# Kernel optimization log

Measured on AMD Instinct MI355X. Metric: run time of the kernel, lower is better.

## Reference

```python
import jax, jax.numpy as jnp
import numpy as np

Q_DEFAULT = 8
XI_MAX = 0.4          # center frequency of the highest-frequency wavelet (cycles/sample)
BW_RATIO = 0.8        # bandwidth-to-center-frequency ratio
LOG_EPS = 1e-6


def _make_filters(T, Q):
    """Morlet-style analytic filter bank in the Fourier domain (all static numpy)."""
    J = int(np.floor(np.log2(T / 2)))
    freqs = np.fft.fftfreq(T).astype(np.float32)          # [T], in [-0.5, 0.5)
    # first-order wavelets: J*Q filters, geometrically spaced, quality factor Q
    n1 = J * Q
    xi1 = (XI_MAX * 2.0 ** (-np.arange(n1) / Q)).astype(np.float32)
    sig1 = (BW_RATIO * xi1 / Q).astype(np.float32)
    psi1 = np.exp(-(freqs[None, :] - xi1[:, None]) ** 2 / (2.0 * sig1[:, None] ** 2)).astype(np.float32)  # [n1, T]
    # second-order wavelets: Q2 = 1, one per octave
    xi2 = (XI_MAX * 2.0 ** (-np.arange(J))).astype(np.float32)
    sig2 = (BW_RATIO * xi2).astype(np.float32)
    psi2 = np.exp(-(freqs[None, :] - xi2[:, None]) ** 2 / (2.0 * sig2[:, None] ** 2)).astype(np.float32)  # [J, T]
    # low-pass (phi): Gaussian at scale 2^J
    sigma_phi = np.float32(BW_RATIO * XI_MAX * 2.0 ** (-J))
    phi = np.exp(-(freqs ** 2) / (2.0 * sigma_phi ** 2)).astype(np.float32)  # [T]
    # valid second-order paths: xi2 strictly below xi1 (frequency-decreasing cascade)
    pair_j1, pair_k = [], []
    for k in range(J):
        for j1 in range(n1):
            if xi2[k] < xi1[j1]:
                pair_j1.append(j1)
                pair_k.append(k)
    return psi1, psi2, phi, np.asarray(pair_j1, np.int32), np.asarray(pair_k, np.int32)


def _scatter(x_flat, psi1, psi2, phi, pair_j1, pair_k):
    """x_flat: [N, T] real. Returns S: [N, 1 + n1 + n_pairs, T]."""
    xh = jnp.fft.fft(x_flat)                                   # [N, T] complex
    S0 = jnp.fft.ifft(xh * phi).real[:, None, :]               # order 0 (dropped later)
    U1 = jnp.abs(jnp.fft.ifft(xh[:, None, :] * psi1[None]))    # [N, n1, T]
    U1h = jnp.fft.fft(U1)
    S1 = jnp.fft.ifft(U1h * phi).real                          # [N, n1, T]
    U2 = jnp.abs(jnp.fft.ifft(U1h[:, pair_j1, :] * psi2[pair_k][None]))  # [N, P, T]
    S2 = jnp.fft.ifft(jnp.fft.fft(U2) * phi).real              # [N, P, T]
    return jnp.concatenate([S0, S1, S2], axis=1)


def setup_inputs() -> dict:
    key = jax.random.key(0)
    x = jax.random.normal(key, (8, 2048, 6), dtype=jnp.float32)
    return {"x": x}


def reference(x):
    B, T, C = x.shape
    psi1, psi2, phi, pj, pk = _make_filters(T, Q_DEFAULT)
    psi1, psi2, phi = jnp.asarray(psi1), jnp.asarray(psi2), jnp.asarray(phi)
    # vectorize the original per-channel Python loop: fold channels into batch
    xf = jnp.transpose(x, (0, 2, 1)).reshape(B * C, T)          # [B*C, T]
    S = _scatter(xf, psi1, psi2, phi, pj, pk)                   # [B*C, n_coef+1, T]
    out = jnp.mean(jnp.log(S[:, 1:, :] + LOG_EPS), axis=-1)     # drop order-0, log, time-mean
    return out.reshape(B, C, -1).transpose(0, 2, 1)             # [B, n_coef, C]
```

## Files before the change

### kernel.cpp

```cpp
#include <hip/hip_runtime.h>

#define NTH 256

#define PHI1 0.29504296f
#define PHI2 0.0075683594f
#define GCUT 18.0f

__device__ __forceinline__ int swz(int i) { return i ^ (((i >> 4) & 3) * 5); }

__device__ __forceinline__ float2 cmul(float2 a, float2 b) {
  return make_float2(a.x * b.x - a.y * b.y, a.x * b.y + a.y * b.x);
}

template <int W>
__device__ __forceinline__ float wsum(float v) {
#pragma unroll
  for (int off = 1; off < W; off <<= 1) v += __shfl_xor(v, off, 64);
  return v;
}

template <int M>
__device__ __forceinline__ int prevM(int i) {
  if (M == 128)
    return ((i >> 5) & 3) | (((i >> 3) & 3) << 2) | (((i >> 1) & 3) << 4) | ((i & 1) << 6);
  else if (M == 256)
    return ((i & 3) << 6) | (((i >> 2) & 3) << 4) | (((i >> 4) & 3) << 2) | ((i >> 6) & 3);
  else if (M == 512)
    return ((i >> 7) & 3) | (((i >> 5) & 3) << 2) | (((i >> 3) & 3) << 4) |
           (((i >> 1) & 3) << 6) | ((i & 1) << 8);
  else if (M == 1024)
    return ((i >> 8) & 3) | (((i >> 6) & 3) << 2) | (((i >> 4) & 3) << 4) |
           (((i >> 2) & 3) << 6) | ((i & 3) << 8);
  else
    return ((i >> 9) & 3) | (((i >> 7) & 3) << 2) | (((i >> 5) & 3) << 4) |
           (((i >> 3) & 3) << 6) | (((i >> 1) & 3) << 8) | ((i & 1) << 10);
}

template <bool INV>
__device__ __forceinline__ void dif4(float2* A, int j, int ls, float astep) {
  const int s = 1 << ls;
  const int e = j & (s - 1);
  const int base = ((j >> ls) << (ls + 2)) | e;
  float2 w1;
  __sincosf(astep * (float)e, &w1.y, &w1.x);
  if (INV) w1.y = -w1.y;
  const float2 w2 = cmul(w1, w1);
  const float2 w3 = cmul(w2, w1);
  const float2 a0 = A[swz(base)];
  const float2 a1 = A[swz(base + s)];
  const float2 a2 = A[swz(base + 2 * s)];
  const float2 a3 = A[swz(base + 3 * s)];
  const float t0x = a0.x + a2.x, t0y = a0.y + a2.y;
  const float t1x = a0.x - a2.x, t1y = a0.y - a2.y;
  const float t2x = a1.x + a3.x, t2y = a1.y + a3.y;
  const float bdx = a1.x - a3.x, bdy = a1.y - a3.y;
  const float sgn = INV ? -1.0f : 1.0f;
  const float t3x = sgn * bdy, t3y = -sgn * bdx;
  A[swz(base)]         = make_float2(t0x + t2x, t0y + t2y);
  A[swz(base + s)]     = cmul(make_float2(t1x + t3x, t1y + t3y), w1);
  A[swz(base + 2 * s)] = cmul(make_float2(t0x - t2x, t0y - t2y), w2);
  A[swz(base + 3 * s)] = cmul(make_float2(t1x - t3x, t1y - t3y), w3);
}

__device__ __forceinline__ void dit4(float2* A, int j, int ls, float astep) {
  const int s = 1 << ls;
  const int e = j & (s - 1);
  const int base = ((j >> ls) << (ls + 2)) | e;
  float2 w1;
  __sincosf(astep * (float)e, &w1.y, &w1.x);
  const float2 w2 = cmul(w1, w1);
  const float2 w3 = cmul(w2, w1);
  const float2 c0 = A[swz(base)];
  const float2 c1 = cmul(A[swz(base + s)], w1);
  const float2 c2 = cmul(A[swz(base + 2 * s)], w2);
  const float2 c3 = cmul(A[swz(base + 3 * s)], w3);
  const float t0x = c0.x + c2.x, t0y = c0.y + c2.y;
  const float t1x = c0.x - c2.x, t1y = c0.y - c2.y;
  const float t2x = c1.x + c3.x, t2y = c1.y + c3.y;
  const float bdx = c1.x - c3.x, bdy = c1.y - c3.y;
  const float t3x = bdy, t3y = -bdx;
  A[swz(base)]         = make_float2(t0x + t2x, t0y + t2y);
  A[swz(base + s)]     = make_float2(t1x + t3x, t1y + t3y);
  A[swz(base + 2 * s)] = make_float2(t0x - t2x, t0y - t2y);
  A[swz(base + 3 * s)] = make_float2(t1x - t3x, t1y - t3y);
}

__device__ __forceinline__ void r2pair(float2* A, int g) {
  const float2 a = A[swz(2 * g)];
  const float2 b = A[swz(2 * g + 1)];
  A[swz(2 * g)]     = make_float2(a.x + b.x, a.y + b.y);
  A[swz(2 * g + 1)] = make_float2(a.x - b.x, a.y - b.y);
}

template <int M> struct LMof { static constexpr int v =
  (M == 2048) ? 11 : (M == 1024) ? 10 : (M == 512) ? 9 : (M == 256) ? 8 : 7; };

template <int M, bool INV>
__device__ __forceinline__ void dif_blk(float2* A) {
  constexpr int LM = LMof<M>::v;
  constexpr int NB = M / 4;
  const int tid = (int)threadIdx.x;
#pragma unroll
  for (int ls = LM - 2; ls >= (LM & 1); ls -= 2) {
    const float astep = -1.5707963267948966f / (float)(1 << ls);
    __syncthreads();
#pragma unroll
    for (int i = 0; i < NB / NTH; ++i) dif4<INV>(A, tid + NTH * i, ls, astep);
  }
  if (LM & 1) {
    __syncthreads();
#pragma unroll
    for (int i = 0; i < (M / 2) / NTH; ++i) r2pair(A, tid + NTH * i);
  }
  __syncthreads();
}

template <int M>
__device__ __forceinline__ void dit_blk(float2* A) {
  constexpr int LM = LMof<M>::v;
  constexpr int NB = M / 4;
  const int tid = (int)threadIdx.x;
  if (LM & 1) {
    __syncthreads();
#pragma unroll
    for (int i = 0; i < (M / 2) / NTH; ++i) r2pair(A, tid + NTH * i);
  }
#pragma unroll
  for (int ls = (LM & 1); ls <= LM - 2; ls += 2) {
    const float astep = -1.5707963267948966f / (float)(1 << ls);
    __syncthreads();
#pragma unroll
    for (int i = 0; i < NB / NTH; ++i) dit4(A, tid + NTH * i, ls, astep);
  }
  __syncthreads();
}

template <int M, bool INV, int LANES>
__device__ __forceinline__ void dif_w(float2* Aw, int l) {
  constexpr int LM = LMof<M>::v;
  constexpr int NB = M / 4;
#pragma unroll
  for (int ls = LM - 2; ls >= (LM & 1); ls -= 2) {
    const float astep = -1.5707963267948966f / (float)(1 << ls);
#pragma unroll
    for (int i = 0; i < NB / LANES; ++i) dif4<INV>(Aw, l + LANES * i, ls, astep);
  }
  if (LM & 1) {
#pragma unroll
    for (int i = 0; i < (M / 2) / LANES; ++i) r2pair(Aw, l + LANES * i);
  }
}

template <int M, int LANES>
__device__ __forceinline__ void dit_w(float2* Aw, int l) {
  constexpr int LM = LMof<M>::v;
  constexpr int NB = M / 4;
  if (LM & 1) {
#pragma unroll
    for (int i = 0; i < (M / 2) / LANES; ++i) r2pair(Aw, l + LANES * i);
  }
#pragma unroll
  for (int ls = (LM & 1); ls <= LM - 2; ls += 2) {
    const float astep = -1.5707963267948966f / (float)(1 << ls);
#pragma unroll
    for (int i = 0; i < NB / LANES; ++i) dit4(Aw, l + LANES * i, ls, astep);
  }
}

__global__ __launch_bounds__(NTH) void kA(const float* __restrict__ x,
                                          float2* __restrict__ xh) {
  __shared__ float2 A[2048];
  const int n = blockIdx.x, b = n / 6, c = n % 6;
  const float* xp = x + (size_t)b * (2048 * 6) + c;
#pragma unroll
  for (int i = 0; i < 8; ++i) {
    const int t = (int)threadIdx.x + NTH * i;
    A[swz(t)] = make_float2(xp[t * 6], 0.0f);
  }
  dif_blk<2048, false>(A);
#pragma unroll
  for (int i = 0; i < 8; ++i) {
    const int t = (int)threadIdx.x + NTH * i;
    xh[(size_t)n * 2048 + prevM<2048>(t)] = A[swz(t)];
  }
}


__device__ __noinline__ void parent_blk1024(const float2* __restrict__ src,
                                            float* __restrict__ outp, int j1) {
  extern __shared__ float2 L[];
  float2* A = L;
  float* scr = (float*)(L + 3968);
  constexpr int M1 = 1024;
  constexpr int NR = 4;
  const int tid = (int)threadIdx.x;
  const float xi = 0.4f * exp2f(-0.125f * (float)j1);
  const float sig = 0.1f * xi;
  const float i2s = 1.0f / (2.0f * sig * sig);
#pragma unroll
  for (int i = 0; i < NR; ++i) {
    const int m = tid + NTH * i;
    float2 acc = make_float2(0.0f, 0.0f);
#pragma unroll
    for (int q = 0; q < 2; ++q) {
      const int f = m + q * M1;
      const float fr = (float)(f < 1024 ? f : f - 2048) * (1.0f / 2048.0f);
      const float d = fr - xi;
      const float dd = d * d * i2s;
      if (dd < GCUT) {
        const float g = __expf(-dd);
        const float2 v = src[f];
        acc.x += v.x * g; acc.y += v.y * g;
      }
    }
    A[swz(m)] = acc;
  }
  dif_blk<M1, true>(A);
#pragma unroll
  for (int i = 0; i < NR; ++i) {
    const int m = tid + NTH * i;
    const float2 zv = A[swz(m)];
    A[swz(m)] = make_float2(sqrtf(zv.x * zv.x + zv.y * zv.y) * (1.0f / 2048.0f), 0.0f);
  }
  dit_blk<M1>(A);
  const float invM = 1.0f / (float)M1;
  const float c0 = A[0].x * invM;
  const float2 U1 = A[1], U2 = A[2];
  const float k1 = PHI1 * 2.0f * invM, k2 = PHI2 * 2.0f * invM;
  float part = 0.0f;
#pragma unroll
  for (int i = 0; i < NR; ++i) {
    const int t = tid + NTH * i;
    float sv, cv;
    __sincosf((6.283185307179586f / (float)M1) * (float)t, &sv, &cv);
    float acc = c0 + k1 * (U1.x * cv - U1.y * sv);
    const float c2 = cv * cv - sv * sv, s2 = 2.0f * sv * cv;
    acc += k2 * (U2.x * c2 - U2.y * s2);
    part += __logf(acc + 1e-6f);
  }
  part = wsum<64>(part);
  const int lane = tid & 63, wid = tid >> 6;
  if (lane == 0) scr[wid] = part;
  __syncthreads();
  if (tid == 0) *outp = (scr[0] + scr[1] + scr[2] + scr[3]) * invM;
}

template <int M1>
__device__ __noinline__ void parent_wav(int aoff, const float2* __restrict__ src,
                                        float* __restrict__ outp, int j1, int l) {
  extern __shared__ float2 L[];
  float2* Aw = L + aoff;
  constexpr int NRW = M1 / 64;
  constexpr int F = 2048 / M1;
  const float xi = 0.4f * exp2f(-0.125f * (float)j1);
  const float sig = 0.1f * xi;
  const float i2s = 1.0f / (2.0f * sig * sig);
#pragma unroll
  for (int i = 0; i < NRW; ++i) {
    const int m = l + 64 * i;
    float2 acc = make_float2(0.0f, 0.0f);
#pragma unroll
    for (int q = 0; q < F; ++q) {
      const int f = m + q * M1;
      const float fr = (float)(f < 1024 ? f : f - 2048) * (1.0f / 2048.0f);
      const float d = fr - xi;
      const float dd = d * d * i2s;
      if (dd < GCUT) {
        const float g = __expf(-dd);
        const float2 v = src[f];
        acc.x += v.x * g; acc.y += v.y * g;
      }
    }
    Aw[swz(m)] = acc;
  }
  dif_w<M1, true, 64>(Aw, l);
#pragma unroll
  for (int i = 0; i < NRW; ++i) {
    const int m = l + 64 * i;
    const float2 zv = Aw[swz(m)];
    Aw[swz(m)] = make_float2(sqrtf(zv.x * zv.x + zv.y * zv.y) * (1.0f / 2048.0f), 0.0f);
  }
  dit_w<M1, 64>(Aw, l);
  const float invM = 1.0f / (float)M1;
  const float c0 = Aw[0].x * invM;
  const float2 U1 = Aw[1], U2 = Aw[2];
  const float k1 = PHI1 * 2.0f * invM, k2 = PHI2 * 2.0f * invM;
  float part = 0.0f;
#pragma unroll
  for (int i = 0; i < NRW; ++i) {
    const int t = l + 64 * i;
    float sv, cv;
    __sincosf((6.283185307179586f / (float)M1) * (float)t, &sv, &cv);
    float acc = c0 + k1 * (U1.x * cv - U1.y * sv);
    const float c2 = cv * cv - sv * sv, s2 = 2.0f * sv * cv;
    acc += k2 * (U2.x * c2 - U2.y * s2);
    part += __logf(acc + 1e-6f);
  }
  part = wsum<64>(part);
  if (l == 0) *outp = part * invM;
}

__device__ __noinline__ void parent_dual(int aoff, const float2* __restrict__ src,
                                         float* __restrict__ outp, int j1, int ll) {
  extern __shared__ float2 L[];
  float2* Ah = L + aoff;
  const float xi = 0.4f * exp2f(-0.125f * (float)j1);
  const float sig = 0.1f * xi;
  const float i2s = 1.0f / (2.0f * sig * sig);
#pragma unroll
  for (int i = 0; i < 4; ++i) {
    const int m = ll + 32 * i;
    float2 acc = make_float2(0.0f, 0.0f);
#pragma unroll
    for (int q = 0; q < 16; ++q) {
      const int f = m + q * 128;
      const float fr = (float)(f < 1024 ? f : f - 2048) * (1.0f / 2048.0f);
      const float d = fr - xi;
      const float dd = d * d * i2s;
      if (dd < GCUT) {
        const float g = __expf(-dd);
        const float2 v = src[f];
        acc.x += v.x * g; acc.y += v.y * g;
      }
    }
    Ah[swz(m)] = acc;
  }
  dif_w<128, true, 32>(Ah, ll);
#pragma unroll
  for (int i = 0; i < 4; ++i) {
    const int m = ll + 32 * i;
    const float2 zv = Ah[swz(m)];
    Ah[swz(m)] = make_float2(sqrtf(zv.x * zv.x + zv.y * zv.y) * (1.0f / 2048.0f), 0.0f);
  }
  dit_w<128, 32>(Ah, ll);
  const float invM = 1.0f / 128.0f;
  const float c0 = Ah[0].x * invM;
  const float2 U1 = Ah[1], U2 = Ah[2];
  const float k1 = PHI1 * 2.0f * invM, k2 = PHI2 * 2.0f * invM;
  float part = 0.0f;
#pragma unroll
  for (int i = 0; i < 4; ++i) {
    const int t = ll + 32 * i;
    float sv, cv;
    __sincosf((6.283185307179586f / 128.0f) * (float)t, &sv, &cv);
    float acc = c0 + k1 * (U1.x * cv - U1.y * sv);
    const float c2 = cv * cv - sv * sv, s2 = 2.0f * sv * cv;
    acc += k2 * (U2.x * c2 - U2.y * s2);
    part += __logf(acc + 1e-6f);
  }
  part = wsum<32>(part);
  if (ll == 0) *outp = part * invM;
}

template <int M2>
__device__ __noinline__ void desc_wav(int aoff, int voff, float* __restrict__ outp,
                                      int M1, int F, float xi, int l) {
  extern __shared__ float2 L[];
  float2* Aw = L + aoff;
  const float2* Vl = L + voff;
  constexpr int NR2 = M2 / 64;
  const float sg = 0.8f * xi;
  const float i2s = 1.0f / (2.0f * sg * sg);
#pragma unroll
  for (int ii = 0; ii < NR2; ++ii) {
    const int m = l + 64 * ii;
    float2 acc = make_float2(0.0f, 0.0f);
    for (int q = 0; q < F; ++q) {
      const int f = m + q * M2;
      const float fr = (float)(f < (M1 >> 1) ? f : f - M1) * (1.0f / 2048.0f);
      const float d = fr - xi;
      const float dd = d * d * i2s;
      if (dd < GCUT) {
        const float g = __expf(-dd);
        const float2 vv = Vl[swz(f)];
        acc.x += vv.x * g; acc.y += vv.y * g;
      }
    }
    Aw[swz(m)] = acc;
  }
  dif_w<M2, true, 64>(Aw, l);
  const float invM1f = 1.0f / (float)M1;
  float b0 = 0, b1r = 0, b1i = 0, b2r = 0, b2i = 0;
#pragma unroll
  for (int ii = 0; ii < NR2; ++ii) {
    const int idx = l + 64 * ii;
    const float2 zv = Aw[swz(idx)];
    const float u = sqrtf(zv.x * zv.x + zv.y * zv.y) * invM1f;
    const int t = prevM<M2>(idx);
    float sv, cv;
    __sincosf((6.283185307179586f / (float)M2) * (float)t, &sv, &cv);
    b0 += u;
    b1r += u * cv; b1i -= u * sv;
    const float c2 = cv * cv - sv * sv, s2 = 2.0f * sv * cv;
    b2r += u * c2; b2i -= u * s2;
  }
  b0 = wsum<64>(b0);
  b1r = wsum<64>(b1r); b1i = wsum<64>(b1i);
  b2r = wsum<64>(b2r); b2i = wsum<64>(b2i);
  const float k1 = 2.0f * PHI1, k2 = 2.0f * PHI2;
  const float invM2 = 1.0f / (float)M2;
  float part = 0.0f;
#pragma unroll
  for (int ii = 0; ii < NR2; ++ii) {
    const int idx = l + 64 * ii;
    const int t = prevM<M2>(idx);
    float sv, cv;
    __sincosf((6.283185307179586f / (float)M2) * (float)t, &sv, &cv);
    float acc = b0 + k1 * (b1r * cv - b1i * sv);
    const float c2 = cv * cv - sv * sv, s2 = 2.0f * sv * cv;
    acc += k2 * (b2r * c2 - b2i * s2);
    part += __logf(acc * invM2 + 1e-6f);
  }
  part = wsum<64>(part);
  if (l == 0) *outp = part * invM2;
}

__device__ __noinline__ void desc_dual(int aoff, int voff, float* __restrict__ outp,
                                       int M1, int F, float xi, int ll) {
  extern __shared__ float2 L[];
  float2* Ah = L + aoff;
  const float2* Vl = L + voff;
  const float sg = 0.8f * xi;
  const float i2s = 1.0f / (2.0f * sg * sg);
#pragma unroll
  for (int ii = 0; ii < 4; ++ii) {
    const int m = ll + 32 * ii;
    float2 acc = make_float2(0.0f, 0.0f);
    for (int q = 0; q < F; ++q) {
      const int f = m + q * 128;
      const float fr = (float)(f < (M1 >> 1) ? f : f - M1) * (1.0f / 2048.0f);
      const float d = fr - xi;
      const float dd = d * d * i2s;
      if (dd < GCUT) {
        const float g = __expf(-dd);
        const float2 vv = Vl[swz(f)];
        acc.x += vv.x * g; acc.y += vv.y * g;
      }
    }
    Ah[swz(m)] = acc;
  }
  dif_w<128, true, 32>(Ah, ll);
  const float invM1f = 1.0f / (float)M1;
  float b0 = 0, b1r = 0, b1i = 0, b2r = 0, b2i = 0;
#pragma unroll
  for (int ii = 0; ii < 4; ++ii) {
    const int idx = ll + 32 * ii;
    const float2 zv = Ah[swz(idx)];
    const float u = sqrtf(zv.x * zv.x + zv.y * zv.y) * invM1f;
    const int t = prevM<128>(idx);
    float sv, cv;
    __sincosf((6.283185307179586f / 128.0f) * (float)t, &sv, &cv);
    b0 += u;
    b1r += u * cv; b1i -= u * sv;
    const float c2 = cv * cv - sv * sv, s2 = 2.0f * sv * cv;
    b2r += u * c2; b2i -= u * s2;
  }
  b0 = wsum<32>(b0);
  b1r = wsum<32>(b1r); b1i = wsum<32>(b1i);
  b2r = wsum<32>(b2r); b2i = wsum<32>(b2i);
  const float k1 = 2.0f * PHI1, k2 = 2.0f * PHI2;
  const float invM2 = 1.0f / 128.0f;
  float part = 0.0f;
#pragma unroll
  for (int ii = 0; ii < 4; ++ii) {
    const int idx = ll + 32 * ii;
    const int t = prevM<128>(idx);
    float sv, cv;
    __sincosf((6.283185307179586f / 128.0f) * (float)t, &sv, &cv);
    float acc = b0 + k1 * (b1r * cv - b1i * sv);
    const float c2 = cv * cv - sv * sv, s2 = 2.0f * sv * cv;
    acc += k2 * (b2r * c2 - b2i * s2);
    part += __logf(acc * invM2 + 1e-6f);
  }
  part = wsum<32>(part);
  if (ll == 0) *outp = part * invM2;
}

__device__ __forceinline__ float* o1p(float* out, int b, int c, int j1) {
  return out + ((size_t)b * 440 + j1) * 6 + c;
}
__device__ __forceinline__ float* o2p(float* out, int b, int c, int j1, int k) {
  return out + ((size_t)b * 440 + 80 + 4 * k * (k - 1) + j1) * 6 + c;
}
__device__ __forceinline__ float xi2f(int k) { return 0.4f * exp2f(-(float)k); }

__global__ __launch_bounds__(NTH, 4) void kBC(const float2* __restrict__ xh,
                                              float* __restrict__ out) {
  extern __shared__ float2 L[];
  const int ci = (int)blockIdx.x / 48;
  const int n  = (int)blockIdx.x % 48;
  const int b = n / 6, c = n % 6;
  const float2* src = xh + (size_t)n * 2048;
  const int tid = (int)threadIdx.x;
  const int wid = tid >> 6, l = tid & 63;
  const int h = l >> 5, ll = l & 31;

  if (ci < 2) {
    const int j1 = 8 + 4 * ci + wid;
    const int a0 = wid * 1024;
    parent_wav<512>(a0, src, o1p(out, b, c, j1), j1, l);
    desc_wav<512>(a0 + 512, a0, o2p(out, b, c, j1, 2), 512, 1, xi2f(2), l);
    desc_wav<256>(a0 + 512, a0, o2p(out, b, c, j1, 3), 512, 2, xi2f(3), l);
    for (int i = 0; i < 3; ++i) {
      const int k = 4 + 2 * i + h;
      desc_dual(a0 + 512 + h * 128, a0, o2p(out, b, c, j1, k), 512, 4, xi2f(k), ll);
    }
  } else if (ci < 4) {
    const int j1 = 16 + 4 * (ci - 2) + wid;
    const int a0 = wid * 512;
    parent_wav<256>(a0, src, o1p(out, b, c, j1), j1, l);
    desc_wav<256>(a0 + 256, a0, o2p(out, b, c, j1, 3), 256, 1, xi2f(3), l);
    for (int i = 0; i < 3; ++i) {
      const int k = 4 + 2 * i + h;
      desc_dual(a0 + 256 + h * 128, a0, o2p(out, b, c, j1, k), 256, 2, xi2f(k), ll);
    }
  } else if (ci < 12) {
    const int j1 = ci - 4;
    parent_blk1024(src, o1p(out, b, c, j1), j1);
    if (wid == 0) {
      desc_wav<1024>(1024, 0, o2p(out, b, c, j1, 1), 1024, 1, xi2f(1), l);
    } else if (wid == 1) {
      desc_wav<512>(2048, 0, o2p(out, b, c, j1, 2), 1024, 2, xi2f(2), l);
      const int k = 5 + h;
      desc_dual(3328 + h * 128, 0, o2p(out, b, c, j1, k), 1024, 8, xi2f(k), ll);
    } else if (wid == 2) {
      desc_wav<512>(2560, 0, o2p(out, b, c, j1, 3), 1024, 2, xi2f(3), l);
      const int k = 7 + h;
      desc_dual(3584 + h * 128, 0, o2p(out, b, c, j1, k), 1024, 8, xi2f(k), ll);
    } else {
      desc_wav<256>(3072, 0, o2p(out, b, c, j1, 4), 1024, 4, xi2f(4), l);
      if (h == 0)
        desc_dual(3840, 0, o2p(out, b, c, j1, 9), 1024, 8, xi2f(9), ll);
    }
  } else {
    const int o = ci - 9;
    const int slot = 2 * wid + h;
    const int j1 = 8 * o + slot;
    const int a0 = slot * 256;
    parent_dual(a0, src, o1p(out, b, c, j1), j1, ll);
    for (int k = o + 1; k <= 9; ++k)
      desc_dual(a0 + 128, a0, o2p(out, b, c, j1, k), 128, 1, xi2f(k), ll);
  }
}

extern "C" void kernel_launch(void* const* d_in, const int* in_sizes, int n_in,
                              void* d_out, int out_size, void* d_ws, size_t ws_size,
                              hipStream_t stream) {
  (void)in_sizes; (void)n_in; (void)out_size; (void)ws_size;
  const float* x = (const float*)d_in[0];
  float* out = (float*)d_out;
  float2* xh = (float2*)d_ws;
  kA<<<dim3(48), dim3(NTH), 0, stream>>>(x, xh);
  kBC<<<dim3(19 * 48), dim3(NTH), 32768, stream>>>(xh, out);
}
```

Baseline: 86.95 us.

## Split scattering into parent and descendant kernels with register-resident shuffle FFTs

Replaces the shared-memory radix-4 FFTs inside the fused second kernel with register-resident FFTs that use in-register butterflies and cross-lane shuffles. The work is split into two kernels: kB computes the first-order wavelet paths and writes U1 spectra to a global workspace, and kC runs each second-order path as its own wave-level task reading from that workspace. This removes shared memory and block barriers and spreads the work across many more blocks to balance load. In exchange it adds a kernel launch and a global round trip for the U1 spectra, and puts more pressure on registers.

```diff
diff --git a/kernel.cpp b/kernel.cpp
--- a/kernel.cpp
+++ b/kernel.cpp
@@ -1,6 +1,7 @@
 #include <hip/hip_runtime.h>
 
 #define NTH 256
+#define U1H_STRIDE 21504
 
 #define PHI1 0.29504296f
 #define PHI2 0.0075683594f
@@ -19,21 +20,75 @@
   return v;
 }
 
-template <int M>
-__device__ __forceinline__ int prevM(int i) {
-  if (M == 128)
-    return ((i >> 5) & 3) | (((i >> 3) & 3) << 2) | (((i >> 1) & 3) << 4) | ((i & 1) << 6);
-  else if (M == 256)
-    return ((i & 3) << 6) | (((i >> 2) & 3) << 4) | (((i >> 4) & 3) << 2) | ((i >> 6) & 3);
-  else if (M == 512)
-    return ((i >> 7) & 3) | (((i >> 5) & 3) << 2) | (((i >> 3) & 3) << 4) |
-           (((i >> 1) & 3) << 6) | ((i & 1) << 8);
-  else if (M == 1024)
-    return ((i >> 8) & 3) | (((i >> 6) & 3) << 2) | (((i >> 4) & 3) << 4) |
-           (((i >> 2) & 3) << 6) | ((i & 3) << 8);
-  else
-    return ((i >> 9) & 3) | (((i >> 7) & 3) << 2) | (((i >> 5) & 3) << 4) |
-           (((i >> 3) & 3) << 6) | (((i >> 1) & 3) << 8) | ((i & 1) << 10);
+__device__ __forceinline__ float2 shflx2(float2 v, int mask) {
+  return make_float2(__shfl_xor(v.x, mask, 64), __shfl_xor(v.y, mask, 64));
+}
+
+template <int M, int LANES, bool INV>
+__device__ __forceinline__ void rdif(float2* x, int l) {
+  constexpr int R = M / LANES;
+#pragma unroll
+  for (int half = R / 2; half >= 1; half >>= 1) {
+    const int s = half * LANES;
+    const float a0 = (INV ? 3.14159265358979f : -3.14159265358979f) / (float)s;
+#pragma unroll
+    for (int r = 0; r < R; ++r) {
+      if ((r & half) == 0) {
+        const float2 a = x[r], b = x[r + half];
+        const int j = (r & (half - 1)) * LANES + l;
+        float2 w; __sincosf(a0 * (float)j, &w.y, &w.x);
+        x[r] = make_float2(a.x + b.x, a.y + b.y);
+        x[r + half] = cmul(make_float2(a.x - b.x, a.y - b.y), w);
+      }
+    }
+  }
+#pragma unroll
+  for (int s = LANES / 2; s >= 1; s >>= 1) {
+    const float a0 = (INV ? 3.14159265358979f : -3.14159265358979f) / (float)s;
+    float2 w; __sincosf(a0 * (float)(l & (s - 1)), &w.y, &w.x);
+    const bool hi = (l & s) != 0;
+#pragma unroll
+    for (int r = 0; r < R; ++r) {
+      const float2 y = shflx2(x[r], s);
+      const float2 sum = make_float2(x[r].x + y.x, x[r].y + y.y);
+      const float2 dif = cmul(make_float2(y.x - x[r].x, y.y - x[r].y), w);
+      x[r] = hi ? dif : sum;
+    }
+  }
+}
+
+template <int M, int LANES, bool INV>
+__device__ __forceinline__ void rdit(float2* x, int l) {
+  constexpr int R = M / LANES;
+#pragma unroll
+  for (int s = 1; s <= LANES / 2; s <<= 1) {
+    const float a0 = (INV ? 3.14159265358979f : -3.14159265358979f) / (float)s;
+    float2 w; __sincosf(a0 * (float)(l & (s - 1)), &w.y, &w.x);
+    const bool hi = (l & s) != 0;
+#pragma unroll
+    for (int r = 0; r < R; ++r) {
+      const float2 y = shflx2(x[r], s);
+      const float2 wb = cmul(w, hi ? x[r] : y);
+      x[r] = hi ? make_float2(y.x - wb.x, y.y - wb.y)
+                : make_float2(x[r].x + wb.x, x[r].y + wb.y);
+    }
+  }
+#pragma unroll
+  for (int half = 1; half <= R / 2; half <<= 1) {
+    const int s = half * LANES;
+    const float a0 = (INV ? 3.14159265358979f : -3.14159265358979f) / (float)s;
+#pragma unroll
+    for (int r = 0; r < R; ++r) {
+      if ((r & half) == 0) {
+        const int j = (r & (half - 1)) * LANES + l;
+        float2 w; __sincosf(a0 * (float)j, &w.y, &w.x);
+        const float2 bw = cmul(x[r + half], w);
+        const float2 a = x[r];
+        x[r] = make_float2(a.x + bw.x, a.y + bw.y);
+        x[r + half] = make_float2(a.x - bw.x, a.y - bw.y);
+      }
+    }
+  }
 }
 
 template <bool INV>
@@ -62,29 +117,6 @@
   A[swz(base + 3 * s)] = cmul(make_float2(t1x - t3x, t1y - t3y), w3);
 }
 
-__device__ __forceinline__ void dit4(float2* A, int j, int ls, float astep) {
-  const int s = 1 << ls;
-  const int e = j & (s - 1);
-  const int base = ((j >> ls) << (ls + 2)) | e;
-  float2 w1;
-  __sincosf(astep * (float)e, &w1.y, &w1.x);
-  const float2 w2 = cmul(w1, w1);
-  const float2 w3 = cmul(w2, w1);
-  const float2 c0 = A[swz(base)];
-  const float2 c1 = cmul(A[swz(base + s)], w1);
-  const float2 c2 = cmul(A[swz(base + 2 * s)], w2);
-  const float2 c3 = cmul(A[swz(base + 3 * s)], w3);
-  const float t0x = c0.x + c2.x, t0y = c0.y + c2.y;
-  const float t1x = c0.x - c2.x, t1y = c0.y - c2.y;
-  const float t2x = c1.x + c3.x, t2y = c1.y + c3.y;
-  const float bdx = c1.x - c3.x, bdy = c1.y - c3.y;
-  const float t3x = bdy, t3y = -bdx;
-  A[swz(base)]         = make_float2(t0x + t2x, t0y + t2y);
-  A[swz(base + s)]     = make_float2(t1x + t3x, t1y + t3y);
-  A[swz(base + 2 * s)] = make_float2(t0x - t2x, t0y - t2y);
-  A[swz(base + 3 * s)] = make_float2(t1x - t3x, t1y - t3y);
-}
-
 __device__ __forceinline__ void r2pair(float2* A, int g) {
   const float2 a = A[swz(2 * g)];
   const float2 b = A[swz(2 * g + 1)];
@@ -92,79 +124,9 @@
   A[swz(2 * g + 1)] = make_float2(a.x - b.x, a.y - b.y);
 }
 
-template <int M> struct LMof { static constexpr int v =
-  (M == 2048) ? 11 : (M == 1024) ? 10 : (M == 512) ? 9 : (M == 256) ? 8 : 7; };
-
-template <int M, bool INV>
-__device__ __forceinline__ void dif_blk(float2* A) {
-  constexpr int LM = LMof<M>::v;
-  constexpr int NB = M / 4;
-  const int tid = (int)threadIdx.x;
-#pragma unroll
-  for (int ls = LM - 2; ls >= (LM & 1); ls -= 2) {
-    const float astep = -1.5707963267948966f / (float)(1 << ls);
-    __syncthreads();
-#pragma unroll
-    for (int i = 0; i < NB / NTH; ++i) dif4<INV>(A, tid + NTH * i, ls, astep);
-  }
-  if (LM & 1) {
-    __syncthreads();
-#pragma unroll
-    for (int i = 0; i < (M / 2) / NTH; ++i) r2pair(A, tid + NTH * i);
-  }
-  __syncthreads();
-}
-
-template <int M>
-__device__ __forceinline__ void dit_blk(float2* A) {
-  constexpr int LM = LMof<M>::v;
-  constexpr int NB = M / 4;
-  const int tid = (int)threadIdx.x;
-  if (LM & 1) {
-    __syncthreads();
-#pragma unroll
-    for (int i = 0; i < (M / 2) / NTH; ++i) r2pair(A, tid + NTH * i);
-  }
-#pragma unroll
-  for (int ls = (LM & 1); ls <= LM - 2; ls += 2) {
-    const float astep = -1.5707963267948966f / (float)(1 << ls);
-    __syncthreads();
-#pragma unroll
-    for (int i = 0; i < NB / NTH; ++i) dit4(A, tid + NTH * i, ls, astep);
-  }
-  __syncthreads();
-}
-
-template <int M, bool INV, int LANES>
-__device__ __forceinline__ void dif_w(float2* Aw, int l) {
-  constexpr int LM = LMof<M>::v;
-  constexpr int NB = M / 4;
-#pragma unroll
-  for (int ls = LM - 2; ls >= (LM & 1); ls -= 2) {
-    const float astep = -1.5707963267948966f / (float)(1 << ls);
-#pragma unroll
-    for (int i = 0; i < NB / LANES; ++i) dif4<INV>(Aw, l + LANES * i, ls, astep);
-  }
-  if (LM & 1) {
-#pragma unroll
-    for (int i = 0; i < (M / 2) / LANES; ++i) r2pair(Aw, l + LANES * i);
-  }
-}
-
-template <int M, int LANES>
-__device__ __forceinline__ void dit_w(float2* Aw, int l) {
-  constexpr int LM = LMof<M>::v;
-  constexpr int NB = M / 4;
-  if (LM & 1) {
-#pragma unroll
-    for (int i = 0; i < (M / 2) / LANES; ++i) r2pair(Aw, l + LANES * i);
-  }
-#pragma unroll
-  for (int ls = (LM & 1); ls <= LM - 2; ls += 2) {
-    const float astep = -1.5707963267948966f / (float)(1 << ls);
-#pragma unroll
-    for (int i = 0; i < NB / LANES; ++i) dit4(Aw, l + LANES * i, ls, astep);
-  }
+__device__ __forceinline__ int prev2048(int i) {
+  return ((i >> 9) & 3) | (((i >> 7) & 3) << 2) | (((i >> 5) & 3) << 4) |
+         (((i >> 3) & 3) << 6) | (((i >> 1) & 3) << 8) | ((i & 1) << 10);
 }
 
 __global__ __launch_bounds__(NTH) void kA(const float* __restrict__ x,
@@ -177,87 +139,56 @@
     const int t = (int)threadIdx.x + NTH * i;
     A[swz(t)] = make_float2(xp[t * 6], 0.0f);
   }
-  dif_blk<2048, false>(A);
+  const int tid = (int)threadIdx.x;
+#pragma unroll
+  for (int ls = 9; ls >= 1; ls -= 2) {
+    const float astep = -1.5707963267948966f / (float)(1 << ls);
+    __syncthreads();
+#pragma unroll
+    for (int i = 0; i < 2; ++i) dif4<false>(A, tid + NTH * i, ls, astep);
+  }
+  __syncthreads();
+#pragma unroll
+  for (int i = 0; i < 4; ++i) r2pair(A, tid + NTH * i);
+  __syncthreads();
 #pragma unroll
   for (int i = 0; i < 8; ++i) {
     const int t = (int)threadIdx.x + NTH * i;
-    xh[(size_t)n * 2048 + prevM<2048>(t)] = A[swz(t)];
-  }
-}
-
-
-__device__ __noinline__ void parent_blk1024(const float2* __restrict__ src,
-                                            float* __restrict__ outp, int j1) {
-  extern __shared__ float2 L[];
-  float2* A = L;
-  float* scr = (float*)(L + 3968);
-  constexpr int M1 = 1024;
-  constexpr int NR = 4;
-  const int tid = (int)threadIdx.x;
+    xh[(size_t)n * 2048 + prev2048(t)] = A[swz(t)];
+  }
+}
+
+__device__ __forceinline__ int u1h_off(int j1) {
+  const int o = j1 >> 3;
+  if (o == 0) return j1 * 1024;
+  if (o == 1) return 8192 + (j1 - 8) * 512;
+  if (o == 2) return 12288 + (j1 - 16) * 256;
+  return 14336 + (j1 - 24) * 128;
+}
+__device__ __forceinline__ float* o1p(float* out, int b, int c, int j1) {
+  return out + ((size_t)b * 440 + j1) * 6 + c;
+}
+__device__ __forceinline__ float* o2p(float* out, int b, int c, int j1, int k) {
+  return out + ((size_t)b * 440 + 80 + 4 * k * (k - 1) + j1) * 6 + c;
+}
+__device__ __forceinline__ float xi2f(int k) { return 0.4f * exp2f(-(float)k); }
+
+template <int M1, int LANES>
+__device__ __forceinline__ void parentR(const float2* __restrict__ src,
+                                        float2* __restrict__ Vg,
+                                        float* __restrict__ outp,
+                                        int j1, int lane) {
+  constexpr int R = M1 / LANES;
+  constexpr int F = 2048 / M1;
+  const int l = lane & (LANES - 1);
+  const int gb = lane - l;
   const float xi = 0.4f * exp2f(-0.125f * (float)j1);
   const float sig = 0.1f * xi;
   const float i2s = 1.0f / (2.0f * sig * sig);
-#pragma unroll
-  for (int i = 0; i < NR; ++i) {
-    const int m = tid + NTH * i;
-    float2 acc = make_float2(0.0f, 0.0f);
-#pragma unroll
-    for (int q = 0; q < 2; ++q) {
-      const int f = m + q * M1;
-      const float fr = (float)(f < 1024 ? f : f - 2048) * (1.0f / 2048.0f);
-      const float d = fr - xi;
-      const float dd = d * d * i2s;
-      if (dd < GCUT) {
-        const float g = __expf(-dd);
-        const float2 v = src[f];
-        acc.x += v.x * g; acc.y += v.y * g;
-      }
-    }
-    A[swz(m)] = acc;
-  }
-  dif_blk<M1, true>(A);
-#pragma unroll
-  for (int i = 0; i < NR; ++i) {
-    const int m = tid + NTH * i;
-    const float2 zv = A[swz(m)];
-    A[swz(m)] = make_float2(sqrtf(zv.x * zv.x + zv.y * zv.y) * (1.0f / 2048.0f), 0.0f);
-  }
-  dit_blk<M1>(A);
-  const float invM = 1.0f / (float)M1;
-  const float c0 = A[0].x * invM;
-  const float2 U1 = A[1], U2 = A[2];
-  const float k1 = PHI1 * 2.0f * invM, k2 = PHI2 * 2.0f * invM;
-  float part = 0.0f;
-#pragma unroll
-  for (int i = 0; i < NR; ++i) {
-    const int t = tid + NTH * i;
-    float sv, cv;
-    __sincosf((6.283185307179586f / (float)M1) * (float)t, &sv, &cv);
-    float acc = c0 + k1 * (U1.x * cv - U1.y * sv);
-    const float c2 = cv * cv - sv * sv, s2 = 2.0f * sv * cv;
-    acc += k2 * (U2.x * c2 - U2.y * s2);
-    part += __logf(acc + 1e-6f);
-  }
-  part = wsum<64>(part);
-  const int lane = tid & 63, wid = tid >> 6;
-  if (lane == 0) scr[wid] = part;
-  __syncthreads();
-  if (tid == 0) *outp = (scr[0] + scr[1] + scr[2] + scr[3]) * invM;
-}
-
-template <int M1>
-__device__ __noinline__ void parent_wav(int aoff, const float2* __restrict__ src,
-                                        float* __restrict__ outp, int j1, int l) {
-  extern __shared__ float2 L[];
-  float2* Aw = L + aoff;
-  constexpr int NRW = M1 / 64;
-  constexpr int F = 2048 / M1;
-  const float xi = 0.4f * exp2f(-0.125f * (float)j1);
-  const float sig = 0.1f * xi;
-  const float i2s = 1.0f / (2.0f * sig * sig);
-#pragma unroll
-  for (int i = 0; i < NRW; ++i) {
-    const int m = l + 64 * i;
+  float2 x[R];
+#pragma unroll
+  for (int r = 0; r < R; ++r) {
+    const int m = r * LANES + l;
     float2 acc = make_float2(0.0f, 0.0f);
 #pragma unroll
     for (int q = 0; q < F; ++q) {
@@ -271,24 +202,24 @@
         acc.x += v.x * g; acc.y += v.y * g;
       }
     }
-    Aw[swz(m)] = acc;
-  }
-  dif_w<M1, true, 64>(Aw, l);
-#pragma unroll
-  for (int i = 0; i < NRW; ++i) {
-    const int m = l + 64 * i;
-    const float2 zv = Aw[swz(m)];
-    Aw[swz(m)] = make_float2(sqrtf(zv.x * zv.x + zv.y * zv.y) * (1.0f / 2048.0f), 0.0f);
-  }
-  dit_w<M1, 64>(Aw, l);
+    x[r] = acc;
+  }
+  rdif<M1, LANES, true>(x, l);
+#pragma unroll
+  for (int r = 0; r < R; ++r)
+    x[r] = make_float2(sqrtf(x[r].x * x[r].x + x[r].y * x[r].y) * (1.0f / 2048.0f), 0.0f);
+  rdit<M1, LANES, false>(x, l);
+#pragma unroll
+  for (int r = 0; r < R; ++r) Vg[r * LANES + l] = x[r];
   const float invM = 1.0f / (float)M1;
-  const float c0 = Aw[0].x * invM;
-  const float2 U1 = Aw[1], U2 = Aw[2];
+  const float c0 = __shfl(x[0].x, gb, 64) * invM;
+  const float2 U1 = make_float2(__shfl(x[0].x, gb + 1, 64), __shfl(x[0].y, gb + 1, 64));
+  const float2 U2 = make_float2(__shfl(x[0].x, gb + 2, 64), __shfl(x[0].y, gb + 2, 64));
   const float k1 = PHI1 * 2.0f * invM, k2 = PHI2 * 2.0f * invM;
   float part = 0.0f;
 #pragma unroll
-  for (int i = 0; i < NRW; ++i) {
-    const int t = l + 64 * i;
+  for (int r = 0; r < R; ++r) {
+    const int t = r * LANES + l;
     float sv, cv;
     __sincosf((6.283185307179586f / (float)M1) * (float)t, &sv, &cv);
     float acc = c0 + k1 * (U1.x * cv - U1.y * sv);
@@ -296,74 +227,51 @@
     acc += k2 * (U2.x * c2 - U2.y * s2);
     part += __logf(acc + 1e-6f);
   }
-  part = wsum<64>(part);
+  part = wsum<LANES>(part);
   if (l == 0) *outp = part * invM;
 }
 
-__device__ __noinline__ void parent_dual(int aoff, const float2* __restrict__ src,
-                                         float* __restrict__ outp, int j1, int ll) {
-  extern __shared__ float2 L[];
-  float2* Ah = L + aoff;
-  const float xi = 0.4f * exp2f(-0.125f * (float)j1);
-  const float sig = 0.1f * xi;
-  const float i2s = 1.0f / (2.0f * sig * sig);
-#pragma unroll
-  for (int i = 0; i < 4; ++i) {
-    const int m = ll + 32 * i;
-    float2 acc = make_float2(0.0f, 0.0f);
-#pragma unroll
-    for (int q = 0; q < 16; ++q) {
-      const int f = m + q * 128;
-      const float fr = (float)(f < 1024 ? f : f - 2048) * (1.0f / 2048.0f);
-      const float d = fr - xi;
-      const float dd = d * d * i2s;
-      if (dd < GCUT) {
-        const float g = __expf(-dd);
-        const float2 v = src[f];
-        acc.x += v.x * g; acc.y += v.y * g;
-      }
-    }
-    Ah[swz(m)] = acc;
-  }
-  dif_w<128, true, 32>(Ah, ll);
-#pragma unroll
-  for (int i = 0; i < 4; ++i) {
-    const int m = ll + 32 * i;
-    const float2 zv = Ah[swz(m)];
-    Ah[swz(m)] = make_float2(sqrtf(zv.x * zv.x + zv.y * zv.y) * (1.0f / 2048.0f), 0.0f);
-  }
-  dit_w<128, 32>(Ah, ll);
-  const float invM = 1.0f / 128.0f;
-  const float c0 = Ah[0].x * invM;
-  const float2 U1 = Ah[1], U2 = Ah[2];
-  const float k1 = PHI1 * 2.0f * invM, k2 = PHI2 * 2.0f * invM;
-  float part = 0.0f;
-#pragma unroll
-  for (int i = 0; i < 4; ++i) {
-    const int t = ll + 32 * i;
-    float sv, cv;
-    __sincosf((6.283185307179586f / 128.0f) * (float)t, &sv, &cv);
-    float acc = c0 + k1 * (U1.x * cv - U1.y * sv);
-    const float c2 = cv * cv - sv * sv, s2 = 2.0f * sv * cv;
-    acc += k2 * (U2.x * c2 - U2.y * s2);
-    part += __logf(acc + 1e-6f);
-  }
-  part = wsum<32>(part);
-  if (ll == 0) *outp = part * invM;
-}
-
-template <int M2>
-__device__ __noinline__ void desc_wav(int aoff, int voff, float* __restrict__ outp,
-                                      int M1, int F, float xi, int l) {
-  extern __shared__ float2 L[];
-  float2* Aw = L + aoff;
-  const float2* Vl = L + voff;
-  constexpr int NR2 = M2 / 64;
+__global__ __launch_bounds__(NTH, 4) void kB(const float2* __restrict__ xh,
+                                             float2* __restrict__ U1h,
+                                             float* __restrict__ out) {
+  const int ci = (int)blockIdx.x / 48;
+  const int n  = (int)blockIdx.x % 48;
+  const int b = n / 6, c = n % 6;
+  const float2* src = xh + (size_t)n * 2048;
+  float2* Vb = U1h + (size_t)n * U1H_STRIDE;
+  const int tid = (int)threadIdx.x;
+  const int wid = tid >> 6, lane = tid & 63;
+  const int h = lane >> 5;
+  const int slot = 2 * wid + h;
+
+  if (ci < 2) {
+    const int j1 = 4 * ci + wid;
+    parentR<1024, 64>(src, Vb + u1h_off(j1), o1p(out, b, c, j1), j1, lane);
+  } else if (ci < 4) {
+    const int j1 = 8 + 4 * (ci - 2) + wid;
+    parentR<512, 64>(src, Vb + u1h_off(j1), o1p(out, b, c, j1), j1, lane);
+  } else if (ci < 6) {
+    const int j1 = 16 + 4 * (ci - 4) + wid;
+    parentR<256, 64>(src, Vb + u1h_off(j1), o1p(out, b, c, j1), j1, lane);
+  } else {
+    const int j1 = 24 + 8 * (ci - 6) + slot;
+    parentR<128, 32>(src, Vb + u1h_off(j1), o1p(out, b, c, j1), j1, lane);
+  }
+}
+
+template <int M2, int LANES>
+__device__ __forceinline__ void descR(const float2* __restrict__ Vg,
+                                      float* __restrict__ outp,
+                                      int M1, int F, float xi, int lane) {
+  constexpr int R = M2 / LANES;
+  constexpr int LM = (M2 == 1024) ? 10 : (M2 == 512) ? 9 : (M2 == 256) ? 8 : 7;
+  const int l = lane & (LANES - 1);
   const float sg = 0.8f * xi;
   const float i2s = 1.0f / (2.0f * sg * sg);
-#pragma unroll
-  for (int ii = 0; ii < NR2; ++ii) {
-    const int m = l + 64 * ii;
+  float2 x[R];
+#pragma unroll
+  for (int r = 0; r < R; ++r) {
+    const int m = r * LANES + l;
     float2 acc = make_float2(0.0f, 0.0f);
     for (int q = 0; q < F; ++q) {
       const int f = m + q * M2;
@@ -372,21 +280,20 @@
       const float dd = d * d * i2s;
       if (dd < GCUT) {
         const float g = __expf(-dd);
-        const float2 vv = Vl[swz(f)];
+        const float2 vv = Vg[f];
         acc.x += vv.x * g; acc.y += vv.y * g;
       }
     }
-    Aw[swz(m)] = acc;
-  }
-  dif_w<M2, true, 64>(Aw, l);
+    x[r] = acc;
+  }
+  rdif<M2, LANES, true>(x, l);
   const float invM1f = 1.0f / (float)M1;
   float b0 = 0, b1r = 0, b1i = 0, b2r = 0, b2i = 0;
 #pragma unroll
-  for (int ii = 0; ii < NR2; ++ii) {
-    const int idx = l + 64 * ii;
-    const float2 zv = Aw[swz(idx)];
-    const float u = sqrtf(zv.x * zv.x + zv.y * zv.y) * invM1f;
-    const int t = prevM<M2>(idx);
+  for (int r = 0; r < R; ++r) {
+    const float u = sqrtf(x[r].x * x[r].x + x[r].y * x[r].y) * invM1f;
+    const int e = r * LANES + l;
+    const int t = (int)(__brev((unsigned)e) >> (32 - LM));
     float sv, cv;
     __sincosf((6.283185307179586f / (float)M2) * (float)t, &sv, &cv);
     b0 += u;
@@ -394,16 +301,16 @@
     const float c2 = cv * cv - sv * sv, s2 = 2.0f * sv * cv;
     b2r += u * c2; b2i -= u * s2;
   }
-  b0 = wsum<64>(b0);
-  b1r = wsum<64>(b1r); b1i = wsum<64>(b1i);
-  b2r = wsum<64>(b2r); b2i = wsum<64>(b2i);
+  b0 = wsum<LANES>(b0);
+  b1r = wsum<LANES>(b1r); b1i = wsum<LANES>(b1i);
+  b2r = wsum<LANES>(b2r); b2i = wsum<LANES>(b2i);
   const float k1 = 2.0f * PHI1, k2 = 2.0f * PHI2;
   const float invM2 = 1.0f / (float)M2;
   float part = 0.0f;
 #pragma unroll
-  for (int ii = 0; ii < NR2; ++ii) {
-    const int idx = l + 64 * ii;
-    const int t = prevM<M2>(idx);
+  for (int r = 0; r < R; ++r) {
+    const int e = r * LANES + l;
+    const int t = (int)(__brev((unsigned)e) >> (32 - LM));
     float sv, cv;
     __sincosf((6.283185307179586f / (float)M2) * (float)t, &sv, &cv);
     float acc = b0 + k1 * (b1r * cv - b1i * sv);
@@ -411,135 +318,50 @@
     acc += k2 * (b2r * c2 - b2i * s2);
     part += __logf(acc * invM2 + 1e-6f);
   }
-  part = wsum<64>(part);
+  part = wsum<LANES>(part);
   if (l == 0) *outp = part * invM2;
 }
 
-__device__ __noinline__ void desc_dual(int aoff, int voff, float* __restrict__ outp,
-                                       int M1, int F, float xi, int ll) {
-  extern __shared__ float2 L[];
-  float2* Ah = L + aoff;
-  const float2* Vl = L + voff;
-  const float sg = 0.8f * xi;
-  const float i2s = 1.0f / (2.0f * sg * sg);
-#pragma unroll
-  for (int ii = 0; ii < 4; ++ii) {
-    const int m = ll + 32 * ii;
-    float2 acc = make_float2(0.0f, 0.0f);
-    for (int q = 0; q < F; ++q) {
-      const int f = m + q * 128;
-      const float fr = (float)(f < (M1 >> 1) ? f : f - M1) * (1.0f / 2048.0f);
-      const float d = fr - xi;
-      const float dd = d * d * i2s;
-      if (dd < GCUT) {
-        const float g = __expf(-dd);
-        const float2 vv = Vl[swz(f)];
-        acc.x += vv.x * g; acc.y += vv.y * g;
-      }
-    }
-    Ah[swz(m)] = acc;
-  }
-  dif_w<128, true, 32>(Ah, ll);
-  const float invM1f = 1.0f / (float)M1;
-  float b0 = 0, b1r = 0, b1i = 0, b2r = 0, b2i = 0;
-#pragma unroll
-  for (int ii = 0; ii < 4; ++ii) {
-    const int idx = ll + 32 * ii;
-    const float2 zv = Ah[swz(idx)];
-    const float u = sqrtf(zv.x * zv.x + zv.y * zv.y) * invM1f;
-    const int t = prevM<128>(idx);
-    float sv, cv;
-    __sincosf((6.283185307179586f / 128.0f) * (float)t, &sv, &cv);
-    b0 += u;
-    b1r += u * cv; b1i -= u * sv;
-    const float c2 = cv * cv - sv * sv, s2 = 2.0f * sv * cv;
-    b2r += u * c2; b2i -= u * s2;
-  }
-  b0 = wsum<32>(b0);
-  b1r = wsum<32>(b1r); b1i = wsum<32>(b1i);
-  b2r = wsum<32>(b2r); b2i = wsum<32>(b2i);
-  const float k1 = 2.0f * PHI1, k2 = 2.0f * PHI2;
-  const float invM2 = 1.0f / 128.0f;
-  float part = 0.0f;
-#pragma unroll
-  for (int ii = 0; ii < 4; ++ii) {
-    const int idx = ll + 32 * ii;
-    const int t = prevM<128>(idx);
-    float sv, cv;
-    __sincosf((6.283185307179586f / 128.0f) * (float)t, &sv, &cv);
-    float acc = b0 + k1 * (b1r * cv - b1i * sv);
-    const float c2 = cv * cv - sv * sv, s2 = 2.0f * sv * cv;
-    acc += k2 * (b2r * c2 - b2i * s2);
-    part += __logf(acc * invM2 + 1e-6f);
-  }
-  part = wsum<32>(part);
-  if (ll == 0) *outp = part * invM2;
-}
-
-__device__ __forceinline__ float* o1p(float* out, int b, int c, int j1) {
-  return out + ((size_t)b * 440 + j1) * 6 + c;
-}
-__device__ __forceinline__ float* o2p(float* out, int b, int c, int j1, int k) {
-  return out + ((size_t)b * 440 + 80 + 4 * k * (k - 1) + j1) * 6 + c;
-}
-__device__ __forceinline__ float xi2f(int k) { return 0.4f * exp2f(-(float)k); }
-
-__global__ __launch_bounds__(NTH, 4) void kBC(const float2* __restrict__ xh,
-                                              float* __restrict__ out) {
-  extern __shared__ float2 L[];
+__global__ __launch_bounds__(NTH, 4) void kC(const float2* __restrict__ U1h,
+                                             float* __restrict__ out) {
   const int ci = (int)blockIdx.x / 48;
   const int n  = (int)blockIdx.x % 48;
   const int b = n / 6, c = n % 6;
-  const float2* src = xh + (size_t)n * 2048;
+  const float2* Vb = U1h + (size_t)n * U1H_STRIDE;
   const int tid = (int)threadIdx.x;
-  const int wid = tid >> 6, l = tid & 63;
-  const int h = l >> 5, ll = l & 31;
+  const int wid = tid >> 6, lane = tid & 63;
+  const int h = lane >> 5;
+  const int slot = 2 * wid + h;
 
   if (ci < 2) {
-    const int j1 = 8 + 4 * ci + wid;
-    const int a0 = wid * 1024;
-    parent_wav<512>(a0, src, o1p(out, b, c, j1), j1, l);
-    desc_wav<512>(a0 + 512, a0, o2p(out, b, c, j1, 2), 512, 1, xi2f(2), l);
-    desc_wav<256>(a0 + 512, a0, o2p(out, b, c, j1, 3), 512, 2, xi2f(3), l);
-    for (int i = 0; i < 3; ++i) {
-      const int k = 4 + 2 * i + h;
-      desc_dual(a0 + 512 + h * 128, a0, o2p(out, b, c, j1, k), 512, 4, xi2f(k), ll);
-    }
-  } else if (ci < 4) {
-    const int j1 = 16 + 4 * (ci - 2) + wid;
-    const int a0 = wid * 512;
-    parent_wav<256>(a0, src, o1p(out, b, c, j1), j1, l);
-    desc_wav<256>(a0 + 256, a0, o2p(out, b, c, j1, 3), 256, 1, xi2f(3), l);
-    for (int i = 0; i < 3; ++i) {
-      const int k = 4 + 2 * i + h;
-      desc_dual(a0 + 256 + h * 128, a0, o2p(out, b, c, j1, k), 256, 2, xi2f(k), ll);
-    }
+    const int j1 = 4 * ci + wid;
+    descR<1024, 64>(Vb + u1h_off(j1), o2p(out, b, c, j1, 1), 1024, 1, xi2f(1), lane);
+  } else if (ci < 6) {
+    const int j1 = 4 * (ci - 2) + wid;
+    const int M1 = (j1 < 8) ? 1024 : 512;
+    descR<512, 64>(Vb + u1h_off(j1), o2p(out, b, c, j1, 2), M1, M1 / 512, xi2f(2), lane);
+  } else if (ci < 8) {
+    const int j1 = 4 * (ci - 6) + wid;
+    descR<512, 64>(Vb + u1h_off(j1), o2p(out, b, c, j1, 3), 1024, 2, xi2f(3), lane);
   } else if (ci < 12) {
-    const int j1 = ci - 4;
-    parent_blk1024(src, o1p(out, b, c, j1), j1);
-    if (wid == 0) {
-      desc_wav<1024>(1024, 0, o2p(out, b, c, j1, 1), 1024, 1, xi2f(1), l);
-    } else if (wid == 1) {
-      desc_wav<512>(2048, 0, o2p(out, b, c, j1, 2), 1024, 2, xi2f(2), l);
-      const int k = 5 + h;
-      desc_dual(3328 + h * 128, 0, o2p(out, b, c, j1, k), 1024, 8, xi2f(k), ll);
-    } else if (wid == 2) {
-      desc_wav<512>(2560, 0, o2p(out, b, c, j1, 3), 1024, 2, xi2f(3), l);
-      const int k = 7 + h;
-      desc_dual(3584 + h * 128, 0, o2p(out, b, c, j1, k), 1024, 8, xi2f(k), ll);
-    } else {
-      desc_wav<256>(3072, 0, o2p(out, b, c, j1, 4), 1024, 4, xi2f(4), l);
-      if (h == 0)
-        desc_dual(3840, 0, o2p(out, b, c, j1, 9), 1024, 8, xi2f(9), ll);
-    }
+    const int j1 = 8 + 4 * (ci - 8) + wid;
+    const int M1 = (j1 < 16) ? 512 : 256;
+    descR<256, 64>(Vb + u1h_off(j1), o2p(out, b, c, j1, 3), M1, M1 / 256, xi2f(3), lane);
+  } else if (ci < 14) {
+    const int j1 = 4 * (ci - 12) + wid;
+    descR<256, 64>(Vb + u1h_off(j1), o2p(out, b, c, j1, 4), 1024, 4, xi2f(4), lane);
+  } else if (ci < 17) {
+    const int j1 = 8 + 8 * (ci - 14) + slot;
+    const int o = j1 >> 3;
+    const int M1 = (o < 3) ? (1024 >> o) : 128;
+    descR<128, 32>(Vb + u1h_off(j1), o2p(out, b, c, j1, 4), M1, M1 / 128, xi2f(4), lane);
   } else {
-    const int o = ci - 9;
-    const int slot = 2 * wid + h;
-    const int j1 = 8 * o + slot;
-    const int a0 = slot * 256;
-    parent_dual(a0, src, o1p(out, b, c, j1), j1, ll);
-    for (int k = o + 1; k <= 9; ++k)
-      desc_dual(a0 + 128, a0, o2p(out, b, c, j1, k), 128, 1, xi2f(k), ll);
+    int g = ci - 17;
+    int k = 5;
+    while (g >= k) { g -= k; ++k; }
+    const int j1 = 8 * g + slot;
+    const int M1 = (g < 3) ? (1024 >> g) : 128;
+    descR<128, 32>(Vb + u1h_off(j1), o2p(out, b, c, j1, k), M1, M1 / 128, xi2f(k), lane);
   }
 }
 
@@ -549,7 +371,9 @@
   (void)in_sizes; (void)n_in; (void)out_size; (void)ws_size;
   const float* x = (const float*)d_in[0];
   float* out = (float*)d_out;
-  float2* xh = (float2*)d_ws;
+  float2* U1h = (float2*)d_ws;
+  float2* xh = (float2*)((char*)d_ws + (size_t)48 * U1H_STRIDE * sizeof(float2));
   kA<<<dim3(48), dim3(NTH), 0, stream>>>(x, xh);
-  kBC<<<dim3(19 * 48), dim3(NTH), 32768, stream>>>(xh, out);
-}
+  kB<<<dim3(13 * 48), dim3(NTH), 0, stream>>>(xh, U1h, out);
+  kC<<<dim3(52 * 48), dim3(NTH), 0, stream>>>(U1h, out);
+}
```

After: 99.50 us. 1.14x slower.
